# Performance work log

Measured on AMD Instinct MI355X. Metric: run time of the kernel, lower is better.

The kernel has to match this reference:

```python
import jax, jax.numpy as jnp
import numpy as np

D_IN = 1024
D_OUT = 1024


def setup_inputs() -> dict:
    key = jax.random.key(0)
    ks = jax.random.split(key, 7)
    s = 1.0 / np.sqrt(D_IN)
    X = jax.random.normal(ks[0], (8, 2048, D_IN), dtype=jnp.float32)
    Wq = jax.random.uniform(ks[1], (D_OUT, D_IN), jnp.float32, -s, s)
    bq = jax.random.uniform(ks[2], (D_OUT,), jnp.float32, -s, s)
    Wk = jax.random.uniform(ks[3], (D_OUT, D_IN), jnp.float32, -s, s)
    bk = jax.random.uniform(ks[4], (D_OUT,), jnp.float32, -s, s)
    Wv = jax.random.uniform(ks[5], (D_OUT, D_IN), jnp.float32, -s, s)
    bv = jax.random.uniform(ks[6], (D_OUT,), jnp.float32, -s, s)
    return {"X": X, "Wq": Wq, "bq": bq, "Wk": Wk, "bk": bk, "Wv": Wv, "bv": bv}


def reference(X, Wq, bq, Wk, bk, Wv, bv):
    # Linear projections (torch Linear: y = x @ W.T + b)
    Q = jnp.einsum('bsi,oi->bso', X, Wq) + bq
    K = jnp.einsum('bsi,oi->bso', X, Wk) + bk
    V = jnp.einsum('bsi,oi->bso', X, Wv) + bv
    # scores[b, j, l] = Q[b, j] . K[b, l]
    scores = jnp.einsum('bjd,bld->bjl', Q, K)
    # FAITHFUL to source: tril zeroes (not -inf) the upper triangle, then scale
    sqrt_dk = jnp.sqrt(jnp.float32(D_OUT))
    scores = jnp.tril(scores) / sqrt_dk
    A = jax.nn.softmax(scores, axis=2)  # [b, j, l]
    # FAITHFUL: einsum 'ijk,ijl->ijl' = sum over k of A, broadcast-multiplied by V
    out = jnp.sum(A, axis=2, keepdims=True) * V  # [b, s, d_out]
    return out
```

## Files before the change

### kernel.cpp

```cpp
#include <hip/hip_runtime.h>
#include <stdint.h>

#define M_TOTAL 16384
#define N_TOTAL 1024
#define K_TOTAL 1024

using f32x4  = __attribute__((ext_vector_type(4))) float;
using bf16x8 = __attribute__((ext_vector_type(8))) short;
using bf16x4 = __attribute__((ext_vector_type(4))) short;

__device__ __forceinline__ unsigned packrne(float x, float y) {
    unsigned ux = __builtin_bit_cast(unsigned, x);
    unsigned uy = __builtin_bit_cast(unsigned, y);
    ux += 0x7fffu + ((ux >> 16) & 1u);
    uy += 0x7fffu + ((uy >> 16) & 1u);
    return (ux >> 16) | (uy & 0xffff0000u);
}

#define N8X (M_TOTAL * K_TOTAL / 8)
#define N8W (N_TOTAL * K_TOTAL / 8)
__global__ __launch_bounds__(256) void cvt2_kernel(
    const float* __restrict__ X, const float* __restrict__ W,
    uint4* __restrict__ Xb, uint4* __restrict__ Wb)
{
    const int i = blockIdx.x * 256 + threadIdx.x;
    const float* src; uint4* dst; int idx;
    if (i < N8X) { src = X; dst = Xb; idx = i; }
    else         { src = W; dst = Wb; idx = i - N8X; }
    const f32x4* p = (const f32x4*)src + (size_t)idx * 2;
    const f32x4 a = p[0], b = p[1];
    uint4 r;
    r.x = packrne(a[0], a[1]);
    r.y = packrne(a[2], a[3]);
    r.z = packrne(b[0], b[1]);
    r.w = packrne(b[2], b[3]);
    dst[idx] = r;
}

#define BM 256
#define BN 256
#define BK 64
#define NTILES (K_TOTAL / BK)
#define NBM (M_TOTAL / BM)
#define NBN (N_TOTAL / BN)
#define NWG (NBM * NBN)

__global__ __launch_bounds__(512) void gemm8_kernel(
    const unsigned short* __restrict__ Xb, const unsigned short* __restrict__ Wb,
    const float* __restrict__ bias, float* __restrict__ C)
{
    __shared__ short smem[65536];

    const int tid  = threadIdx.x;
    const int lane = tid & 63;
    const int wave = tid >> 6;
    const int wr = wave >> 2;
    const int wc = wave & 3;

    const int bid  = blockIdx.x;
    const int work = (bid & 7) * (NWG / 8) + (bid >> 3);
    const int bm = work >> 2;
    const int bn = work & 3;
    const int m0 = bm * BM, n0 = bn * BN;

    const int srow64 = wave * 8 + (lane >> 3);
    const int kge    = ((lane & 7) ^ ((lane >> 3) & 7)) * 8;

    f32x4 acc[8][4] = {};

    auto stage_tile = [&](int t, int dbuf) {
        const int k0 = t * BK;
        #pragma unroll
        for (int j = 0; j < 4; ++j) {
            __builtin_amdgcn_global_load_lds(
                (const __attribute__((address_space(1))) void*)
                    (Xb + (size_t)(m0 + j * 64 + srow64) * K_TOTAL + k0 + kge),
                (__attribute__((address_space(3))) void*)
                    ((char*)smem + dbuf * 32768 + j * 8192 + wave * 1024),
                16, 0, 0);
        }
        #pragma unroll
        for (int j = 0; j < 4; ++j) {
            __builtin_amdgcn_global_load_lds(
                (const __attribute__((address_space(1))) void*)
                    (Wb + (size_t)(n0 + j * 64 + srow64) * K_TOTAL + k0 + kge),
                (__attribute__((address_space(3))) void*)
                    ((char*)smem + 65536 + dbuf * 32768 + j * 8192 + wave * 1024),
                16, 0, 0);
        }
    };

    const int cl = lane & 15;
    const int kb = lane >> 4;

    auto compute_tile = [&](int dbuf) {
        const char* Abase = (const char*)smem + dbuf * 32768;
        const char* Bbase = (const char*)smem + 65536 + dbuf * 32768;
        bf16x8 aF[4][2], bF0[2][2], bF1[2][2];

        #pragma unroll
        for (int i = 0; i < 4; ++i) {
            const int ar = wr * 128 + i * 16 + cl;
            const int rs = ar & 7;
            aF[i][0] = *(const bf16x8*)(Abase + ar * 128 + ((kb       ^ rs) << 4));
            aF[i][1] = *(const bf16x8*)(Abase + ar * 128 + (((kb + 4) ^ rs) << 4));
        }
        #pragma unroll
        for (int j = 0; j < 2; ++j) {
            const int br = wc * 64 + j * 16 + cl;
            const int rs = br & 7;
            bF0[j][0] = *(const bf16x8*)(Bbase + br * 128 + ((kb       ^ rs) << 4));
            bF0[j][1] = *(const bf16x8*)(Bbase + br * 128 + (((kb + 4) ^ rs) << 4));
        }
        __builtin_amdgcn_s_setprio(1);
        #pragma unroll
        for (int i = 0; i < 4; ++i)
            #pragma unroll
            for (int j = 0; j < 2; ++j) {
                acc[i][j] = __builtin_amdgcn_mfma_f32_16x16x32_bf16(aF[i][0], bF0[j][0], acc[i][j], 0, 0, 0);
                acc[i][j] = __builtin_amdgcn_mfma_f32_16x16x32_bf16(aF[i][1], bF0[j][1], acc[i][j], 0, 0, 0);
            }
        __builtin_amdgcn_s_setprio(0);

        #pragma unroll
        for (int j = 0; j < 2; ++j) {
            const int br = wc * 64 + 32 + j * 16 + cl;
            const int rs = br & 7;
            bF1[j][0] = *(const bf16x8*)(Bbase + br * 128 + ((kb       ^ rs) << 4));
            bF1[j][1] = *(const bf16x8*)(Bbase + br * 128 + (((kb + 4) ^ rs) << 4));
        }
        __builtin_amdgcn_s_setprio(1);
        #pragma unroll
        for (int i = 0; i < 4; ++i)
            #pragma unroll
            for (int j = 0; j < 2; ++j) {
                acc[i][2 + j] = __builtin_amdgcn_mfma_f32_16x16x32_bf16(aF[i][0], bF1[j][0], acc[i][2 + j], 0, 0, 0);
                acc[i][2 + j] = __builtin_amdgcn_mfma_f32_16x16x32_bf16(aF[i][1], bF1[j][1], acc[i][2 + j], 0, 0, 0);
            }
        __builtin_amdgcn_s_setprio(0);

        #pragma unroll
        for (int i = 0; i < 4; ++i) {
            const int ar = wr * 128 + 64 + i * 16 + cl;
            const int rs = ar & 7;
            aF[i][0] = *(const bf16x8*)(Abase + ar * 128 + ((kb       ^ rs) << 4));
            aF[i][1] = *(const bf16x8*)(Abase + ar * 128 + (((kb + 4) ^ rs) << 4));
        }
        __builtin_amdgcn_s_setprio(1);
        #pragma unroll
        for (int i = 0; i < 4; ++i)
            #pragma unroll
            for (int j = 0; j < 2; ++j) {
                acc[4 + i][2 + j] = __builtin_amdgcn_mfma_f32_16x16x32_bf16(aF[i][0], bF1[j][0], acc[4 + i][2 + j], 0, 0, 0);
                acc[4 + i][2 + j] = __builtin_amdgcn_mfma_f32_16x16x32_bf16(aF[i][1], bF1[j][1], acc[4 + i][2 + j], 0, 0, 0);
            }
        __builtin_amdgcn_s_setprio(0);

        __builtin_amdgcn_s_setprio(1);
        #pragma unroll
        for (int i = 0; i < 4; ++i)
            #pragma unroll
            for (int j = 0; j < 2; ++j) {
                acc[4 + i][j] = __builtin_amdgcn_mfma_f32_16x16x32_bf16(aF[i][0], bF0[j][0], acc[4 + i][j], 0, 0, 0);
                acc[4 + i][j] = __builtin_amdgcn_mfma_f32_16x16x32_bf16(aF[i][1], bF0[j][1], acc[4 + i][j], 0, 0, 0);
            }
        __builtin_amdgcn_s_setprio(0);
    };

    stage_tile(0, 0);
    #pragma unroll 1
    for (int t = 0; t < NTILES - 1; ++t) {
        const int d = t & 1;
        __builtin_amdgcn_sched_barrier(0);
        __builtin_amdgcn_s_barrier();
        __builtin_amdgcn_sched_barrier(0);
        stage_tile(t + 1, d ^ 1);
        asm volatile("s_waitcnt vmcnt(8)" ::: "memory");
        __builtin_amdgcn_sched_barrier(0);
        __builtin_amdgcn_s_barrier();
        __builtin_amdgcn_sched_barrier(0);
        compute_tile(d);
    }
    __builtin_amdgcn_sched_barrier(0);
    asm volatile("s_waitcnt vmcnt(0)" ::: "memory");
    __builtin_amdgcn_s_barrier();
    __builtin_amdgcn_sched_barrier(0);
    compute_tile(1);

    const int r0 = (lane >> 4) * 4;
    #pragma unroll
    for (int ni = 0; ni < 4; ++ni) {
        const int n = n0 + wc * 64 + ni * 16 + cl;
        const float bvv = bias[n];
        #pragma unroll
        for (int mi = 0; mi < 8; ++mi) {
            const int m = m0 + wr * 128 + mi * 16 + r0;
            #pragma unroll
            for (int r = 0; r < 4; ++r)
                C[(size_t)(m + r) * N_TOTAL + n] = acc[mi][ni][r] + bvv;
        }
    }
}

__device__ __forceinline__ short f2bf(float f) {
    unsigned u = __builtin_bit_cast(unsigned, f);
    u += 0x7fffu + ((u >> 16) & 1u);
    return (short)(u >> 16);
}

#define FBM 128
#define FBN 128
#define FNWG ((M_TOTAL / FBM) * (N_TOTAL / FBN))

__global__ __launch_bounds__(256) void fb_gemm_bias_kernel(
    const float* __restrict__ X, const float* __restrict__ W,
    const float* __restrict__ bias, float* __restrict__ C)
{
    __shared__ short As[FBM * BK];
    __shared__ short Bs[FBN * BK];

    const int tid  = threadIdx.x;
    const int lane = tid & 63;
    const int wave = tid >> 6;
    const int wr = wave >> 1;
    const int wc = wave & 1;

    const int bid  = blockIdx.x;
    const int work = (bid & 7) * (FNWG / 8) + (bid >> 3);
    const int bm = work >> 3;
    const int bn = work & 7;
    const int m0 = bm * FBM, n0 = bn * FBN;

    const int srow  = tid >> 4;
    const int scol4 = tid & 15;

    f32x4 acc[4][4] = {};
    char* const Ab = (char*)As;
    char* const Bb = (char*)Bs;

    for (int k0 = 0; k0 < K_TOTAL; k0 += BK) {
        __syncthreads();
        #pragma unroll
        for (int pass = 0; pass < 8; ++pass) {
            const int row = srow + pass * 16;
            const int off = (row * (BK * 2) + scol4 * 8) ^ ((row & 7) << 4);
            {
                const f32x4 v = *(const f32x4*)(X + (size_t)(m0 + row) * K_TOTAL + k0 + scol4 * 4);
                bf16x4 b;
                b[0] = f2bf(v[0]); b[1] = f2bf(v[1]); b[2] = f2bf(v[2]); b[3] = f2bf(v[3]);
                *(bf16x4*)(Ab + off) = b;
            }
            {
                const f32x4 v = *(const f32x4*)(W + (size_t)(n0 + row) * K_TOTAL + k0 + scol4 * 4);
                bf16x4 b;
                b[0] = f2bf(v[0]); b[1] = f2bf(v[1]); b[2] = f2bf(v[2]); b[3] = f2bf(v[3]);
                *(bf16x4*)(Bb + off) = b;
            }
        }
        __syncthreads();

        #pragma unroll
        for (int ks = 0; ks < 2; ++ks) {
            const int kel = ks * 32 + ((lane >> 4) << 3);
            bf16x8 af[4], bfr[4];
            #pragma unroll
            for (int i = 0; i < 4; ++i) {
                const int arow = wr * 64 + i * 16 + (lane & 15);
                af[i]  = *(const bf16x8*)(Ab + ((arow * (BK * 2) + kel * 2) ^ ((arow & 7) << 4)));
                const int brow = wc * 64 + i * 16 + (lane & 15);
                bfr[i] = *(const bf16x8*)(Bb + ((brow * (BK * 2) + kel * 2) ^ ((brow & 7) << 4)));
            }
            #pragma unroll
            for (int mi = 0; mi < 4; ++mi)
                #pragma unroll
                for (int ni = 0; ni < 4; ++ni)
                    acc[mi][ni] = __builtin_amdgcn_mfma_f32_16x16x32_bf16(
                        af[mi], bfr[ni], acc[mi][ni], 0, 0, 0);
        }
    }

    const int cl = lane & 15;
    const int r0 = (lane >> 4) * 4;
    #pragma unroll
    for (int ni = 0; ni < 4; ++ni) {
        const int n = n0 + wc * 64 + ni * 16 + cl;
        const float bvv = bias[n];
        #pragma unroll
        for (int mi = 0; mi < 4; ++mi) {
            const int m = m0 + wr * 64 + mi * 16 + r0;
            #pragma unroll
            for (int r = 0; r < 4; ++r)
                C[(size_t)(m + r) * N_TOTAL + n] = acc[mi][ni][r] + bvv;
        }
    }
}

extern "C" void kernel_launch(void* const* d_in, const int* in_sizes, int n_in,
                              void* d_out, int out_size, void* d_ws, size_t ws_size,
                              hipStream_t stream) {
    const float* X  = (const float*)d_in[0];
    const float* Wv = (const float*)d_in[5];
    const float* bv = (const float*)d_in[6];
    float* out = (float*)d_out;

    const size_t XB_BYTES = (size_t)M_TOTAL * K_TOTAL * 2;
    const size_t WB_BYTES = (size_t)N_TOTAL * K_TOTAL * 2;

    if (ws_size >= XB_BYTES + WB_BYTES) {
        unsigned short* Xb = (unsigned short*)d_ws;
        unsigned short* Wb = (unsigned short*)((char*)d_ws + XB_BYTES);
        cvt2_kernel<<<dim3((N8X + N8W) / 256), dim3(256), 0, stream>>>(
            X, Wv, (uint4*)Xb, (uint4*)Wb);
        gemm8_kernel<<<dim3(NWG), dim3(512), 0, stream>>>(Xb, Wb, bv, out);
    } else {
        fb_gemm_bias_kernel<<<dim3(FNWG), dim3(256), 0, stream>>>(X, Wv, bv, out);
    }
}
```

Before: 62.09 us.

## Pre-swizzle weights into MFMA fragment layout and load B directly to registers

The conversion kernel now writes the bf16 weight matrix in a fragment-ordered layout, so each wave can load its B operands straight from global memory into registers with coalesced 16-byte loads, skipping LDS staging for B. LDS is halved to hold only A tiles, and launch bounds request two blocks per CU. The main loop is restructured to prefetch B one tile ahead in registers and stage A two tiles ahead. The costs are higher register pressure from double-buffered B fragments, which may clash with the occupancy target, and redundant global reads of B across the waves that share a column.

New measurement: 64.20 us. +3.4%, slower.

```diff
diff --git a/kernel.cpp b/kernel.cpp
--- a/kernel.cpp
+++ b/kernel.cpp
@@ -18,23 +18,38 @@
 }
 
 #define N8X (M_TOTAL * K_TOTAL / 8)
-#define N8W (N_TOTAL * K_TOTAL / 8)
+#define NWF (N_TOTAL * K_TOTAL / 8)
 __global__ __launch_bounds__(256) void cvt2_kernel(
     const float* __restrict__ X, const float* __restrict__ W,
-    uint4* __restrict__ Xb, uint4* __restrict__ Wb)
+    uint4* __restrict__ Xb, uint4* __restrict__ Wf)
 {
     const int i = blockIdx.x * 256 + threadIdx.x;
-    const float* src; uint4* dst; int idx;
-    if (i < N8X) { src = X; dst = Xb; idx = i; }
-    else         { src = W; dst = Wb; idx = i - N8X; }
-    const f32x4* p = (const f32x4*)src + (size_t)idx * 2;
-    const f32x4 a = p[0], b = p[1];
-    uint4 r;
-    r.x = packrne(a[0], a[1]);
-    r.y = packrne(a[2], a[3]);
-    r.z = packrne(b[0], b[1]);
-    r.w = packrne(b[2], b[3]);
-    dst[idx] = r;
+    if (i < N8X) {
+        const f32x4* p = (const f32x4*)X + (size_t)i * 2;
+        const f32x4 a = p[0], b = p[1];
+        uint4 r;
+        r.x = packrne(a[0], a[1]);
+        r.y = packrne(a[2], a[3]);
+        r.z = packrne(b[0], b[1]);
+        r.w = packrne(b[2], b[3]);
+        Xb[i] = r;
+    } else {
+        const int idx = i - N8X;
+        const int J  = idx >> 11;
+        const int rem = idx & 2047;
+        const int h  = rem >> 6;
+        const int l  = rem & 63;
+        const int cl = l & 15, kb = l >> 4;
+        const float* src = W + (size_t)(J * 16 + cl) * K_TOTAL + h * 32 + kb * 8;
+        const f32x4 a = *(const f32x4*)src;
+        const f32x4 b = *(const f32x4*)(src + 4);
+        uint4 r;
+        r.x = packrne(a[0], a[1]);
+        r.y = packrne(a[2], a[3]);
+        r.z = packrne(b[0], b[1]);
+        r.w = packrne(b[2], b[3]);
+        Wf[idx] = r;
+    }
 }
 
 #define BM 256
@@ -45,11 +60,11 @@
 #define NBN (N_TOTAL / BN)
 #define NWG (NBM * NBN)
 
-__global__ __launch_bounds__(512) void gemm8_kernel(
-    const unsigned short* __restrict__ Xb, const unsigned short* __restrict__ Wb,
+__global__ __launch_bounds__(512, 2) void gemm8_kernel(
+    const unsigned short* __restrict__ Xb, const unsigned short* __restrict__ Wfu,
     const float* __restrict__ bias, float* __restrict__ C)
 {
-    __shared__ short smem[65536];
+    __shared__ short smem[2 * 16384];
 
     const int tid  = threadIdx.x;
     const int lane = tid & 63;
@@ -66,9 +81,7 @@
     const int srow64 = wave * 8 + (lane >> 3);
     const int kge    = ((lane & 7) ^ ((lane >> 3) & 7)) * 8;
 
-    f32x4 acc[8][4] = {};
-
-    auto stage_tile = [&](int t, int dbuf) {
+    auto stage_A = [&](int t, int buf) {
         const int k0 = t * BK;
         #pragma unroll
         for (int j = 0; j < 4; ++j) {
@@ -76,28 +89,39 @@
                 (const __attribute__((address_space(1))) void*)
                     (Xb + (size_t)(m0 + j * 64 + srow64) * K_TOTAL + k0 + kge),
                 (__attribute__((address_space(3))) void*)
-                    ((char*)smem + dbuf * 32768 + j * 8192 + wave * 1024),
+                    ((char*)smem + buf * 32768 + j * 8192 + wave * 1024),
                 16, 0, 0);
         }
-        #pragma unroll
-        for (int j = 0; j < 4; ++j) {
-            __builtin_amdgcn_global_load_lds(
-                (const __attribute__((address_space(1))) void*)
-                    (Wb + (size_t)(n0 + j * 64 + srow64) * K_TOTAL + k0 + kge),
-                (__attribute__((address_space(3))) void*)
-                    ((char*)smem + 65536 + dbuf * 32768 + j * 8192 + wave * 1024),
-                16, 0, 0);
-        }
+    };
+
+    const uint4* Wf = (const uint4*)Wfu;
+    const int Jbase = (n0 + wc * 64) >> 4;
+
+    auto load_B = [&](int t, bf16x8 (&B)[4][2]) {
+        #pragma unroll
+        for (int jj = 0; jj < 4; ++jj)
+            #pragma unroll
+            for (int hh = 0; hh < 2; ++hh)
+                B[jj][hh] = __builtin_bit_cast(bf16x8,
+                    Wf[(size_t)(Jbase + jj) * 2048 + (t * 2 + hh) * 64 + lane]);
     };
 
     const int cl = lane & 15;
     const int kb = lane >> 4;
 
-    auto compute_tile = [&](int dbuf) {
-        const char* Abase = (const char*)smem + dbuf * 32768;
-        const char* Bbase = (const char*)smem + 65536 + dbuf * 32768;
-        bf16x8 aF[4][2], bF0[2][2], bF1[2][2];
-
+    f32x4 acc[8][4] = {};
+
+    auto iter_body = [&](int t, bf16x8 (&Bcur)[4][2], bf16x8 (&Bnxt)[4][2]) {
+        const int buf = t & 1;
+        asm volatile("s_waitcnt vmcnt(8)" ::: "memory");
+        __builtin_amdgcn_sched_barrier(0);
+        __builtin_amdgcn_s_barrier();
+        __builtin_amdgcn_sched_barrier(0);
+
+        if (t + 1 < NTILES) load_B(t + 1, Bnxt);
+
+        const char* Abase = (const char*)smem + buf * 32768;
+        bf16x8 aF[4][2];
         #pragma unroll
         for (int i = 0; i < 4; ++i) {
             const int ar = wr * 128 + i * 16 + cl;
@@ -105,40 +129,15 @@
             aF[i][0] = *(const bf16x8*)(Abase + ar * 128 + ((kb       ^ rs) << 4));
             aF[i][1] = *(const bf16x8*)(Abase + ar * 128 + (((kb + 4) ^ rs) << 4));
         }
-        #pragma unroll
-        for (int j = 0; j < 2; ++j) {
-            const int br = wc * 64 + j * 16 + cl;
-            const int rs = br & 7;
-            bF0[j][0] = *(const bf16x8*)(Bbase + br * 128 + ((kb       ^ rs) << 4));
-            bF0[j][1] = *(const bf16x8*)(Bbase + br * 128 + (((kb + 4) ^ rs) << 4));
-        }
         __builtin_amdgcn_s_setprio(1);
         #pragma unroll
         for (int i = 0; i < 4; ++i)
             #pragma unroll
-            for (int j = 0; j < 2; ++j) {
-                acc[i][j] = __builtin_amdgcn_mfma_f32_16x16x32_bf16(aF[i][0], bF0[j][0], acc[i][j], 0, 0, 0);
-                acc[i][j] = __builtin_amdgcn_mfma_f32_16x16x32_bf16(aF[i][1], bF0[j][1], acc[i][j], 0, 0, 0);
+            for (int jj = 0; jj < 4; ++jj) {
+                acc[i][jj] = __builtin_amdgcn_mfma_f32_16x16x32_bf16(aF[i][0], Bcur[jj][0], acc[i][jj], 0, 0, 0);
+                acc[i][jj] = __builtin_amdgcn_mfma_f32_16x16x32_bf16(aF[i][1], Bcur[jj][1], acc[i][jj], 0, 0, 0);
             }
         __builtin_amdgcn_s_setprio(0);
-
-        #pragma unroll
-        for (int j = 0; j < 2; ++j) {
-            const int br = wc * 64 + 32 + j * 16 + cl;
-            const int rs = br & 7;
-            bF1[j][0] = *(const bf16x8*)(Bbase + br * 128 + ((kb       ^ rs) << 4));
-            bF1[j][1] = *(const bf16x8*)(Bbase + br * 128 + (((kb + 4) ^ rs) << 4));
-        }
-        __builtin_amdgcn_s_setprio(1);
-        #pragma unroll
-        for (int i = 0; i < 4; ++i)
-            #pragma unroll
-            for (int j = 0; j < 2; ++j) {
-                acc[i][2 + j] = __builtin_amdgcn_mfma_f32_16x16x32_bf16(aF[i][0], bF1[j][0], acc[i][2 + j], 0, 0, 0);
-                acc[i][2 + j] = __builtin_amdgcn_mfma_f32_16x16x32_bf16(aF[i][1], bF1[j][1], acc[i][2 + j], 0, 0, 0);
-            }
-        __builtin_amdgcn_s_setprio(0);
-
         #pragma unroll
         for (int i = 0; i < 4; ++i) {
             const int ar = wr * 128 + 64 + i * 16 + cl;
@@ -150,42 +149,27 @@
         #pragma unroll
         for (int i = 0; i < 4; ++i)
             #pragma unroll
-            for (int j = 0; j < 2; ++j) {
-                acc[4 + i][2 + j] = __builtin_amdgcn_mfma_f32_16x16x32_bf16(aF[i][0], bF1[j][0], acc[4 + i][2 + j], 0, 0, 0);
-                acc[4 + i][2 + j] = __builtin_amdgcn_mfma_f32_16x16x32_bf16(aF[i][1], bF1[j][1], acc[4 + i][2 + j], 0, 0, 0);
+            for (int jj = 0; jj < 4; ++jj) {
+                acc[4 + i][jj] = __builtin_amdgcn_mfma_f32_16x16x32_bf16(aF[i][0], Bcur[jj][0], acc[4 + i][jj], 0, 0, 0);
+                acc[4 + i][jj] = __builtin_amdgcn_mfma_f32_16x16x32_bf16(aF[i][1], Bcur[jj][1], acc[4 + i][jj], 0, 0, 0);
             }
         __builtin_amdgcn_s_setprio(0);
 
-        __builtin_amdgcn_s_setprio(1);
-        #pragma unroll
-        for (int i = 0; i < 4; ++i)
-            #pragma unroll
-            for (int j = 0; j < 2; ++j) {
-                acc[4 + i][j] = __builtin_amdgcn_mfma_f32_16x16x32_bf16(aF[i][0], bF0[j][0], acc[4 + i][j], 0, 0, 0);
-                acc[4 + i][j] = __builtin_amdgcn_mfma_f32_16x16x32_bf16(aF[i][1], bF0[j][1], acc[4 + i][j], 0, 0, 0);
-            }
-        __builtin_amdgcn_s_setprio(0);
-    };
-
-    stage_tile(0, 0);
-    #pragma unroll 1
-    for (int t = 0; t < NTILES - 1; ++t) {
-        const int d = t & 1;
         __builtin_amdgcn_sched_barrier(0);
         __builtin_amdgcn_s_barrier();
         __builtin_amdgcn_sched_barrier(0);
-        stage_tile(t + 1, d ^ 1);
-        asm volatile("s_waitcnt vmcnt(8)" ::: "memory");
-        __builtin_amdgcn_sched_barrier(0);
-        __builtin_amdgcn_s_barrier();
-        __builtin_amdgcn_sched_barrier(0);
-        compute_tile(d);
-    }
-    __builtin_amdgcn_sched_barrier(0);
-    asm volatile("s_waitcnt vmcnt(0)" ::: "memory");
-    __builtin_amdgcn_s_barrier();
-    __builtin_amdgcn_sched_barrier(0);
-    compute_tile(1);
+        if (t + 2 < NTILES) stage_A(t + 2, buf);
+    };
+
+    bf16x8 B0r[4][2], B1r[4][2];
+    load_B(0, B0r);
+    stage_A(0, 0);
+    stage_A(1, 1);
+    #pragma unroll 1
+    for (int t = 0; t < NTILES; t += 2) {
+        iter_body(t,     B0r, B1r);
+        iter_body(t + 1, B1r, B0r);
+    }
 
     const int r0 = (lane >> 4) * 4;
     #pragma unroll
@@ -304,14 +288,14 @@
     float* out = (float*)d_out;
 
     const size_t XB_BYTES = (size_t)M_TOTAL * K_TOTAL * 2;
-    const size_t WB_BYTES = (size_t)N_TOTAL * K_TOTAL * 2;
-
-    if (ws_size >= XB_BYTES + WB_BYTES) {
+    const size_t WF_BYTES = (size_t)N_TOTAL * K_TOTAL * 2;
+
+    if (ws_size >= XB_BYTES + WF_BYTES) {
         unsigned short* Xb = (unsigned short*)d_ws;
-        unsigned short* Wb = (unsigned short*)((char*)d_ws + XB_BYTES);
-        cvt2_kernel<<<dim3((N8X + N8W) / 256), dim3(256), 0, stream>>>(
-            X, Wv, (uint4*)Xb, (uint4*)Wb);
-        gemm8_kernel<<<dim3(NWG), dim3(512), 0, stream>>>(Xb, Wb, bv, out);
+        unsigned short* Wf = (unsigned short*)((char*)d_ws + XB_BYTES);
+        cvt2_kernel<<<dim3((N8X + NWF) / 256), dim3(256), 0, stream>>>(
+            X, Wv, (uint4*)Xb, (uint4*)Wf);
+        gemm8_kernel<<<dim3(NWG), dim3(512), 0, stream>>>(Xb, Wf, bv, out);
     } else {
         fb_gemm_bias_kernel<<<dim3(FNWG), dim3(256), 0, stream>>>(X, Wv, bv, out);
     }
```

## Split GEMM tile staging into quarter phases interleaved with MFMA blocks

Applied to the files above, without the earlier changes.

Restructures the bf16 GEMM main loop into four phases per K tile. Each phase issues one half-tile global->LDS load for the next tile, reads fragments and runs one quarter of the MFMAs, with explicit barriers and vmcnt/lgkmcnt waits between phases. The LDS layout is reordered so each half of A and B is contiguous per phase. The aim is to overlap global loads with compute more finely, at the cost of many more workgroup barriers per tile.

Measured after the change: 60.61 us. 1.02x faster.

```diff
diff --git a/kernel.cpp b/kernel.cpp
--- a/kernel.cpp
+++ b/kernel.cpp
@@ -8,6 +8,10 @@
 using f32x4  = __attribute__((ext_vector_type(4))) float;
 using bf16x8 = __attribute__((ext_vector_type(8))) short;
 using bf16x4 = __attribute__((ext_vector_type(4))) short;
+
+#define AS1 __attribute__((address_space(1)))
+#define AS3 __attribute__((address_space(3)))
+#define SB() __builtin_amdgcn_sched_barrier(0)
 
 __device__ __forceinline__ unsigned packrne(float x, float y) {
     unsigned ux = __builtin_bit_cast(unsigned, x);
@@ -45,11 +49,11 @@
 #define NBN (N_TOTAL / BN)
 #define NWG (NBM * NBN)
 
-__global__ __launch_bounds__(512) void gemm8_kernel(
+__global__ __launch_bounds__(512) void gemm8p_kernel(
     const unsigned short* __restrict__ Xb, const unsigned short* __restrict__ Wb,
     const float* __restrict__ bias, float* __restrict__ C)
 {
-    __shared__ short smem[65536];
+    __shared__ __align__(16) char smem[131072];
 
     const int tid  = threadIdx.x;
     const int lane = tid & 63;
@@ -63,129 +67,115 @@
     const int bn = work & 3;
     const int m0 = bm * BM, n0 = bn * BN;
 
-    const int srow64 = wave * 8 + (lane >> 3);
-    const int kge    = ((lane & 7) ^ ((lane >> 3) & 7)) * 8;
-
-    f32x4 acc[8][4] = {};
-
-    auto stage_tile = [&](int t, int dbuf) {
-        const int k0 = t * BK;
-        #pragma unroll
-        for (int j = 0; j < 4; ++j) {
+    const int kge = (((lane & 7) ^ ((lane >> 3) & 7)) << 3);
+
+    auto stage_A = [&](int tt, int b, int ha) {
+        #pragma unroll
+        for (int j = 0; j < 2; ++j) {
+            const int qb  = ha * 128 + wave * 16 + j * 8;
+            const int row = ((qb >> 6) & 1) * 128 + ha * 64 + (qb & 63) + (lane >> 3);
             __builtin_amdgcn_global_load_lds(
-                (const __attribute__((address_space(1))) void*)
-                    (Xb + (size_t)(m0 + j * 64 + srow64) * K_TOTAL + k0 + kge),
-                (__attribute__((address_space(3))) void*)
-                    ((char*)smem + dbuf * 32768 + j * 8192 + wave * 1024),
-                16, 0, 0);
-        }
-        #pragma unroll
-        for (int j = 0; j < 4; ++j) {
+                (const AS1 void*)(Xb + (size_t)(m0 + row) * K_TOTAL + tt * BK + kge),
+                (AS3 void*)(smem + b * 32768 + qb * 128), 16, 0, 0);
+        }
+    };
+    auto stage_B = [&](int tt, int b, int hb) {
+        #pragma unroll
+        for (int j = 0; j < 2; ++j) {
+            const int pb  = hb * 128 + wave * 16 + j * 8;
+            const int col = ((pb >> 5) & 3) * 64 + hb * 32 + (pb & 31) + (lane >> 3);
             __builtin_amdgcn_global_load_lds(
-                (const __attribute__((address_space(1))) void*)
-                    (Wb + (size_t)(n0 + j * 64 + srow64) * K_TOTAL + k0 + kge),
-                (__attribute__((address_space(3))) void*)
-                    ((char*)smem + 65536 + dbuf * 32768 + j * 8192 + wave * 1024),
-                16, 0, 0);
+                (const AS1 void*)(Wb + (size_t)(n0 + col) * K_TOTAL + tt * BK + kge),
+                (AS3 void*)(smem + 65536 + b * 32768 + pb * 128), 16, 0, 0);
         }
     };
 
     const int cl = lane & 15;
     const int kb = lane >> 4;
-
-    auto compute_tile = [&](int dbuf) {
-        const char* Abase = (const char*)smem + dbuf * 32768;
-        const char* Bbase = (const char*)smem + 65536 + dbuf * 32768;
-        bf16x8 aF[4][2], bF0[2][2], bF1[2][2];
-
+    const int sw = cl & 7;
+
+    bf16x8 aF[4][2], bLo[2][2], bHi[2][2];
+    f32x4 acc[8][4] = {};
+
+    auto read_A = [&](int b, int ha) {
+        const char* Ab = smem + b * 32768;
         #pragma unroll
         for (int i = 0; i < 4; ++i) {
-            const int ar = wr * 128 + i * 16 + cl;
-            const int rs = ar & 7;
-            aF[i][0] = *(const bf16x8*)(Abase + ar * 128 + ((kb       ^ rs) << 4));
-            aF[i][1] = *(const bf16x8*)(Abase + ar * 128 + (((kb + 4) ^ rs) << 4));
-        }
+            const int q = ha * 128 + wr * 64 + i * 16 + cl;
+            aF[i][0] = *(const bf16x8*)(Ab + q * 128 + ((kb       ^ sw) << 4));
+            aF[i][1] = *(const bf16x8*)(Ab + q * 128 + (((kb + 4) ^ sw) << 4));
+        }
+    };
+    auto read_B = [&](int b, int hb, bf16x8 (&B)[2][2]) {
+        const char* Bb = smem + 65536 + b * 32768;
         #pragma unroll
         for (int j = 0; j < 2; ++j) {
-            const int br = wc * 64 + j * 16 + cl;
-            const int rs = br & 7;
-            bF0[j][0] = *(const bf16x8*)(Bbase + br * 128 + ((kb       ^ rs) << 4));
-            bF0[j][1] = *(const bf16x8*)(Bbase + br * 128 + (((kb + 4) ^ rs) << 4));
-        }
-        __builtin_amdgcn_s_setprio(1);
-        #pragma unroll
-        for (int i = 0; i < 4; ++i)
-            #pragma unroll
-            for (int j = 0; j < 2; ++j) {
-                acc[i][j] = __builtin_amdgcn_mfma_f32_16x16x32_bf16(aF[i][0], bF0[j][0], acc[i][j], 0, 0, 0);
-                acc[i][j] = __builtin_amdgcn_mfma_f32_16x16x32_bf16(aF[i][1], bF0[j][1], acc[i][j], 0, 0, 0);
-            }
-        __builtin_amdgcn_s_setprio(0);
-
-        #pragma unroll
-        for (int j = 0; j < 2; ++j) {
-            const int br = wc * 64 + 32 + j * 16 + cl;
-            const int rs = br & 7;
-            bF1[j][0] = *(const bf16x8*)(Bbase + br * 128 + ((kb       ^ rs) << 4));
-            bF1[j][1] = *(const bf16x8*)(Bbase + br * 128 + (((kb + 4) ^ rs) << 4));
-        }
-        __builtin_amdgcn_s_setprio(1);
-        #pragma unroll
-        for (int i = 0; i < 4; ++i)
-            #pragma unroll
-            for (int j = 0; j < 2; ++j) {
-                acc[i][2 + j] = __builtin_amdgcn_mfma_f32_16x16x32_bf16(aF[i][0], bF1[j][0], acc[i][2 + j], 0, 0, 0);
-                acc[i][2 + j] = __builtin_amdgcn_mfma_f32_16x16x32_bf16(aF[i][1], bF1[j][1], acc[i][2 + j], 0, 0, 0);
-            }
-        __builtin_amdgcn_s_setprio(0);
-
-        #pragma unroll
-        for (int i = 0; i < 4; ++i) {
-            const int ar = wr * 128 + 64 + i * 16 + cl;
-            const int rs = ar & 7;
-            aF[i][0] = *(const bf16x8*)(Abase + ar * 128 + ((kb       ^ rs) << 4));
-            aF[i][1] = *(const bf16x8*)(Abase + ar * 128 + (((kb + 4) ^ rs) << 4));
-        }
-        __builtin_amdgcn_s_setprio(1);
-        #pragma unroll
-        for (int i = 0; i < 4; ++i)
-            #pragma unroll
-            for (int j = 0; j < 2; ++j) {
-                acc[4 + i][2 + j] = __builtin_amdgcn_mfma_f32_16x16x32_bf16(aF[i][0], bF1[j][0], acc[4 + i][2 + j], 0, 0, 0);
-                acc[4 + i][2 + j] = __builtin_amdgcn_mfma_f32_16x16x32_bf16(aF[i][1], bF1[j][1], acc[4 + i][2 + j], 0, 0, 0);
-            }
-        __builtin_amdgcn_s_setprio(0);
-
-        __builtin_amdgcn_s_setprio(1);
-        #pragma unroll
-        for (int i = 0; i < 4; ++i)
-            #pragma unroll
-            for (int j = 0; j < 2; ++j) {
-                acc[4 + i][j] = __builtin_amdgcn_mfma_f32_16x16x32_bf16(aF[i][0], bF0[j][0], acc[4 + i][j], 0, 0, 0);
-                acc[4 + i][j] = __builtin_amdgcn_mfma_f32_16x16x32_bf16(aF[i][1], bF0[j][1], acc[4 + i][j], 0, 0, 0);
-            }
-        __builtin_amdgcn_s_setprio(0);
+            const int p = hb * 128 + wc * 32 + j * 16 + cl;
+            B[j][0] = *(const bf16x8*)(Bb + p * 128 + ((kb       ^ sw) << 4));
+            B[j][1] = *(const bf16x8*)(Bb + p * 128 + (((kb + 4) ^ sw) << 4));
+        }
     };
 
-    stage_tile(0, 0);
+#define MFMA_Q(MI0, NI0, BREG)                                                      \
+    __builtin_amdgcn_s_setprio(1);                                                  \
+    _Pragma("unroll")                                                               \
+    for (int i = 0; i < 4; ++i) {                                                   \
+        _Pragma("unroll")                                                           \
+        for (int j = 0; j < 2; ++j) {                                               \
+            acc[(MI0) + i][(NI0) + j] = __builtin_amdgcn_mfma_f32_16x16x32_bf16(    \
+                aF[i][0], BREG[j][0], acc[(MI0) + i][(NI0) + j], 0, 0, 0);          \
+            acc[(MI0) + i][(NI0) + j] = __builtin_amdgcn_mfma_f32_16x16x32_bf16(    \
+                aF[i][1], BREG[j][1], acc[(MI0) + i][(NI0) + j], 0, 0, 0);          \
+        }                                                                           \
+    }                                                                               \
+    __builtin_amdgcn_s_setprio(0);
+
+#define BARRIER() SB(); __builtin_amdgcn_s_barrier(); SB()
+#define LGKM0()   asm volatile("s_waitcnt lgkmcnt(0)" ::: "memory"); SB()
+#define VM(N)     asm volatile("s_waitcnt vmcnt(" #N ")" ::: "memory"); SB()
+
+    stage_A(0, 0, 0);
+    stage_B(0, 0, 0);
+    stage_B(0, 0, 1);
+    stage_A(0, 0, 1);
+    VM(4);
+    BARRIER();
+
     #pragma unroll 1
-    for (int t = 0; t < NTILES - 1; ++t) {
-        const int d = t & 1;
-        __builtin_amdgcn_sched_barrier(0);
-        __builtin_amdgcn_s_barrier();
-        __builtin_amdgcn_sched_barrier(0);
-        stage_tile(t + 1, d ^ 1);
-        asm volatile("s_waitcnt vmcnt(8)" ::: "memory");
-        __builtin_amdgcn_sched_barrier(0);
-        __builtin_amdgcn_s_barrier();
-        __builtin_amdgcn_sched_barrier(0);
-        compute_tile(d);
-    }
-    __builtin_amdgcn_sched_barrier(0);
-    asm volatile("s_waitcnt vmcnt(0)" ::: "memory");
-    __builtin_amdgcn_s_barrier();
-    __builtin_amdgcn_sched_barrier(0);
-    compute_tile(1);
+    for (int t = 0; t < NTILES; ++t) {
+        const int buf = t & 1, nbuf = buf ^ 1;
+        const bool nx = (t + 1 < NTILES);
+
+        read_A(buf, 0);
+        read_B(buf, 0, bLo);
+        if (nx) stage_A(t + 1, nbuf, 0);
+        BARRIER();
+        LGKM0();
+        MFMA_Q(0, 0, bLo);
+        if (nx) { VM(4); } else { VM(2); }
+        BARRIER();
+
+        read_B(buf, 1, bHi);
+        if (nx) stage_B(t + 1, nbuf, 0);
+        BARRIER();
+        LGKM0();
+        MFMA_Q(0, 2, bHi);
+        if (nx) { VM(4); } else { VM(0); }
+        BARRIER();
+
+        read_A(buf, 1);
+        if (nx) stage_B(t + 1, nbuf, 1);
+        BARRIER();
+        LGKM0();
+        MFMA_Q(4, 2, bHi);
+        BARRIER();
+
+        if (nx) stage_A(t + 1, nbuf, 1);
+        BARRIER();
+        MFMA_Q(4, 0, bLo);
+        if (nx) { VM(4); }
+        BARRIER();
+    }
 
     const int r0 = (lane >> 4) * 4;
     #pragma unroll
@@ -200,6 +190,10 @@
                 C[(size_t)(m + r) * N_TOTAL + n] = acc[mi][ni][r] + bvv;
         }
     }
+#undef MFMA_Q
+#undef BARRIER
+#undef LGKM0
+#undef VM
 }
 
 __device__ __forceinline__ short f2bf(float f) {
@@ -311,7 +305,7 @@
         unsigned short* Wb = (unsigned short*)((char*)d_ws + XB_BYTES);
         cvt2_kernel<<<dim3((N8X + N8W) / 256), dim3(256), 0, stream>>>(
             X, Wv, (uint4*)Xb, (uint4*)Wb);
-        gemm8_kernel<<<dim3(NWG), dim3(512), 0, stream>>>(Xb, Wb, bv, out);
+        gemm8p_kernel<<<dim3(NWG), dim3(512), 0, stream>>>(Xb, Wb, bv, out);
     } else {
         fb_gemm_bias_kernel<<<dim3(FNWG), dim3(256), 0, stream>>>(X, Wv, bv, out);
     }
```

## Fuse X fp32-to-bf16 conversion into GEMM A-tile staging with register prefetch

Applied to the files above, without the earlier changes.

Drops the separate pass that converted all of X to bf16 in workspace. The GEMM now loads fp32 X rows into registers, prefetched one tile ahead, and packs them to bf16 before storing them swizzled into LDS. Only W is still pre-converted and loaded with direct global-to-LDS loads. This saves the extra write and re-read of a 32MB bf16 copy of X, but each GEMM block now reads fp32 X four times (once per N-block), and the kernel uses more registers and synchronisation to stage A.

Result: slower. 137.3 us (+121.1%).

```diff
diff --git a/kernel.cpp b/kernel.cpp
--- a/kernel.cpp
+++ b/kernel.cpp
@@ -4,10 +4,19 @@
 #define M_TOTAL 16384
 #define N_TOTAL 1024
 #define K_TOTAL 1024
+#define BM 256
+#define BN 256
+#define BK 64
+#define NTILES (K_TOTAL / BK)
+#define NWG ((M_TOTAL / BM) * (N_TOTAL / BN))
 
 using f32x4  = __attribute__((ext_vector_type(4))) float;
 using bf16x8 = __attribute__((ext_vector_type(8))) short;
 using bf16x4 = __attribute__((ext_vector_type(4))) short;
+
+#define AS1 __attribute__((address_space(1)))
+#define AS3 __attribute__((address_space(3)))
+#define SB() __builtin_amdgcn_sched_barrier(0)
 
 __device__ __forceinline__ unsigned packrne(float x, float y) {
     unsigned ux = __builtin_bit_cast(unsigned, x);
@@ -17,39 +26,26 @@
     return (ux >> 16) | (uy & 0xffff0000u);
 }
 
-#define N8X (M_TOTAL * K_TOTAL / 8)
 #define N8W (N_TOTAL * K_TOTAL / 8)
-__global__ __launch_bounds__(256) void cvt2_kernel(
-    const float* __restrict__ X, const float* __restrict__ W,
-    uint4* __restrict__ Xb, uint4* __restrict__ Wb)
+__global__ __launch_bounds__(256) void cvtW_kernel(
+    const float* __restrict__ W, uint4* __restrict__ Wb)
 {
     const int i = blockIdx.x * 256 + threadIdx.x;
-    const float* src; uint4* dst; int idx;
-    if (i < N8X) { src = X; dst = Xb; idx = i; }
-    else         { src = W; dst = Wb; idx = i - N8X; }
-    const f32x4* p = (const f32x4*)src + (size_t)idx * 2;
+    const f32x4* p = (const f32x4*)W + (size_t)i * 2;
     const f32x4 a = p[0], b = p[1];
     uint4 r;
     r.x = packrne(a[0], a[1]);
     r.y = packrne(a[2], a[3]);
     r.z = packrne(b[0], b[1]);
     r.w = packrne(b[2], b[3]);
-    dst[idx] = r;
-}
-
-#define BM 256
-#define BN 256
-#define BK 64
-#define NTILES (K_TOTAL / BK)
-#define NBM (M_TOTAL / BM)
-#define NBN (N_TOTAL / BN)
-#define NWG (NBM * NBN)
-
-__global__ __launch_bounds__(512) void gemm8_kernel(
-    const unsigned short* __restrict__ Xb, const unsigned short* __restrict__ Wb,
+    Wb[i] = r;
+}
+
+__global__ __launch_bounds__(512) void gemm8f_kernel(
+    const float* __restrict__ X, const unsigned short* __restrict__ Wb,
     const float* __restrict__ bias, float* __restrict__ C)
 {
-    __shared__ short smem[65536];
+    __shared__ __align__(16) char smem[131072];
 
     const int tid  = threadIdx.x;
     const int lane = tid & 63;
@@ -65,37 +61,52 @@
 
     const int srow64 = wave * 8 + (lane >> 3);
     const int kge    = ((lane & 7) ^ ((lane >> 3) & 7)) * 8;
-
-    f32x4 acc[8][4] = {};
-
-    auto stage_tile = [&](int t, int dbuf) {
-        const int k0 = t * BK;
+    auto stage_B = [&](int t, int b) {
         #pragma unroll
         for (int j = 0; j < 4; ++j) {
             __builtin_amdgcn_global_load_lds(
-                (const __attribute__((address_space(1))) void*)
-                    (Xb + (size_t)(m0 + j * 64 + srow64) * K_TOTAL + k0 + kge),
-                (__attribute__((address_space(3))) void*)
-                    ((char*)smem + dbuf * 32768 + j * 8192 + wave * 1024),
+                (const AS1 void*)(Wb + (size_t)(n0 + j * 64 + srow64) * K_TOTAL
+                                     + t * BK + kge),
+                (AS3 void*)(smem + 65536 + b * 32768 + j * 8192 + wave * 1024),
                 16, 0, 0);
         }
+    };
+
+    const int arow = tid >> 1;
+    const int ac   = tid & 1;
+    const int ars  = arow & 7;
+    auto load_A = [&](int t, f32x4 (&v)[8]) {
+        const f32x4* p = (const f32x4*)(X + (size_t)(m0 + arow) * K_TOTAL
+                                          + t * BK + ac * 32);
+        #pragma unroll
+        for (int i = 0; i < 8; ++i) v[i] = p[i];
+    };
+    auto write_A = [&](int b, const f32x4 (&v)[8]) {
         #pragma unroll
         for (int j = 0; j < 4; ++j) {
-            __builtin_amdgcn_global_load_lds(
-                (const __attribute__((address_space(1))) void*)
-                    (Wb + (size_t)(n0 + j * 64 + srow64) * K_TOTAL + k0 + kge),
-                (__attribute__((address_space(3))) void*)
-                    ((char*)smem + 65536 + dbuf * 32768 + j * 8192 + wave * 1024),
-                16, 0, 0);
+            uint4 c;
+            c.x = packrne(v[2 * j][0], v[2 * j][1]);
+            c.y = packrne(v[2 * j][2], v[2 * j][3]);
+            c.z = packrne(v[2 * j + 1][0], v[2 * j + 1][1]);
+            c.w = packrne(v[2 * j + 1][2], v[2 * j + 1][3]);
+            *(uint4*)(smem + b * 32768 + arow * 128
+                      + (((ac * 4 + j) ^ ars) << 4)) = c;
         }
     };
 
     const int cl = lane & 15;
     const int kb = lane >> 4;
 
-    auto compute_tile = [&](int dbuf) {
-        const char* Abase = (const char*)smem + dbuf * 32768;
-        const char* Bbase = (const char*)smem + 65536 + dbuf * 32768;
+    f32x4 acc[8][4] = {};
+
+#define BARRIER() SB(); __builtin_amdgcn_s_barrier(); SB()
+#define LGKM0()   asm volatile("s_waitcnt lgkmcnt(0)" ::: "memory"); SB()
+#define VM0()     asm volatile("s_waitcnt vmcnt(0)" ::: "memory"); SB()
+
+    auto compute_tile = [&](int dbuf, f32x4 (&L)[8], bool doload, int tload) {
+        if (doload) load_A(tload, L);
+        const char* Abase = smem + dbuf * 32768;
+        const char* Bbase = smem + 65536 + dbuf * 32768;
         bf16x8 aF[4][2], bF0[2][2], bF1[2][2];
 
         #pragma unroll
@@ -167,25 +178,33 @@
         __builtin_amdgcn_s_setprio(0);
     };
 
-    stage_tile(0, 0);
+    f32x4 aP[8], aQ[8];
+    stage_B(0, 0);
+    load_A(0, aP);
+    load_A(1, aQ);
+    write_A(0, aP);
+    LGKM0();
+
     #pragma unroll 1
-    for (int t = 0; t < NTILES - 1; ++t) {
-        const int d = t & 1;
-        __builtin_amdgcn_sched_barrier(0);
-        __builtin_amdgcn_s_barrier();
-        __builtin_amdgcn_sched_barrier(0);
-        stage_tile(t + 1, d ^ 1);
-        asm volatile("s_waitcnt vmcnt(8)" ::: "memory");
-        __builtin_amdgcn_sched_barrier(0);
-        __builtin_amdgcn_s_barrier();
-        __builtin_amdgcn_sched_barrier(0);
-        compute_tile(d);
-    }
-    __builtin_amdgcn_sched_barrier(0);
-    asm volatile("s_waitcnt vmcnt(0)" ::: "memory");
-    __builtin_amdgcn_s_barrier();
-    __builtin_amdgcn_sched_barrier(0);
-    compute_tile(1);
+    for (int t = 0; t < NTILES; t += 2) {
+        BARRIER();
+        write_A(1, aQ);
+        stage_B(t + 1, 1);
+        LGKM0();
+        BARRIER();
+        compute_tile(0, aP, t + 2 < NTILES, t + 2);
+
+        BARRIER();
+        if (t + 2 < NTILES) {
+            write_A(0, aP);
+            stage_B(t + 2, 0);
+            LGKM0();
+        } else {
+            VM0();
+        }
+        BARRIER();
+        compute_tile(1, aQ, t + 3 < NTILES, t + 3);
+    }
 
     const int r0 = (lane >> 4) * 4;
     #pragma unroll
@@ -200,6 +219,9 @@
                 C[(size_t)(m + r) * N_TOTAL + n] = acc[mi][ni][r] + bvv;
         }
     }
+#undef BARRIER
+#undef LGKM0
+#undef VM0
 }
 
 __device__ __forceinline__ short f2bf(float f) {
@@ -265,10 +287,10 @@
             bf16x8 af[4], bfr[4];
             #pragma unroll
             for (int i = 0; i < 4; ++i) {
-                const int arow = wr * 64 + i * 16 + (lane & 15);
-                af[i]  = *(const bf16x8*)(Ab + ((arow * (BK * 2) + kel * 2) ^ ((arow & 7) << 4)));
-                const int brow = wc * 64 + i * 16 + (lane & 15);
-                bfr[i] = *(const bf16x8*)(Bb + ((brow * (BK * 2) + kel * 2) ^ ((brow & 7) << 4)));
+                const int ar = wr * 64 + i * 16 + (lane & 15);
+                af[i]  = *(const bf16x8*)(Ab + ((ar * (BK * 2) + kel * 2) ^ ((ar & 7) << 4)));
+                const int br = wc * 64 + i * 16 + (lane & 15);
+                bfr[i] = *(const bf16x8*)(Bb + ((br * (BK * 2) + kel * 2) ^ ((br & 7) << 4)));
             }
             #pragma unroll
             for (int mi = 0; mi < 4; ++mi)
@@ -303,15 +325,12 @@
     const float* bv = (const float*)d_in[6];
     float* out = (float*)d_out;
 
-    const size_t XB_BYTES = (size_t)M_TOTAL * K_TOTAL * 2;
     const size_t WB_BYTES = (size_t)N_TOTAL * K_TOTAL * 2;
 
-    if (ws_size >= XB_BYTES + WB_BYTES) {
-        unsigned short* Xb = (unsigned short*)d_ws;
-        unsigned short* Wb = (unsigned short*)((char*)d_ws + XB_BYTES);
-        cvt2_kernel<<<dim3((N8X + N8W) / 256), dim3(256), 0, stream>>>(
-            X, Wv, (uint4*)Xb, (uint4*)Wb);
-        gemm8_kernel<<<dim3(NWG), dim3(512), 0, stream>>>(Xb, Wb, bv, out);
+    if (ws_size >= WB_BYTES) {
+        unsigned short* Wb = (unsigned short*)d_ws;
+        cvtW_kernel<<<dim3(N8W / 256), dim3(256), 0, stream>>>(Wv, (uint4*)Wb);
+        gemm8f_kernel<<<dim3(NWG), dim3(512), 0, stream>>>(X, Wb, bv, out);
     } else {
         fb_gemm_bias_kernel<<<dim3(FNWG), dim3(256), 0, stream>>>(X, Wv, bv, out);
     }
```
